# Kernel tuning notes

Measured on AMD Instinct MI355X. Metric: run time of the kernel, lower is better.

## Reference

```python
import jax, jax.numpy as jnp
import numpy as np
import math

D = 768
H = 12
HD = D // H  # 64
B, N = 16, 1024
EPS = 1e-5


def _rope(x, cos, sin):
    # x: [B,N,H,hd]; cos,sin: [1,N,1,hd]
    x1, x2 = x[..., ::2], x[..., 1::2]
    return jnp.concatenate(
        [x1 * cos[..., ::2] - x2 * sin[..., ::2],
         x1 * sin[..., 1::2] + x2 * cos[..., 1::2]], axis=-1)


def setup_inputs() -> dict:
    key = jax.random.key(0)
    ks = jax.random.split(key, 8)
    s = 1.0 / math.sqrt(D)  # xavier-ish scale
    return {
        "x": jax.random.normal(ks[0], (B, N, D), jnp.float32),
        "rope_emb": jax.random.normal(ks[1], (N, HD), jnp.float32),
        "ln_w": jnp.ones((D,), jnp.float32),
        "ln_b": jnp.zeros((D,), jnp.float32),
        "enc_w": jax.random.normal(ks[2], (D, D), jnp.float32) * s,
        "enc_b": jnp.zeros((D,), jnp.float32),
        "qk_w": jax.random.normal(ks[3], (D, D), jnp.float32) * s,
        "qk_b": jnp.zeros((D,), jnp.float32),
        "v_w": jax.random.normal(ks[4], (D, D), jnp.float32) * s,
        "v_b": jnp.zeros((D,), jnp.float32),
        "out_w": jax.random.normal(ks[5], (D, D), jnp.float32) * s,
        "out_b": jnp.zeros((D,), jnp.float32),
        "gate_w": jax.random.normal(ks[6], (D, D), jnp.float32) * s,
        "gate_b": jnp.zeros((D,), jnp.float32),
    }


def reference(x, rope_emb, ln_w, ln_b, enc_w, enc_b, qk_w, qk_b,
              v_w, v_b, out_w, out_b, gate_w, gate_b):
    b, n, d = x.shape
    # Pre-LayerNorm
    mu = jnp.mean(x, axis=-1, keepdims=True)
    var = jnp.mean(jnp.square(x - mu), axis=-1, keepdims=True)
    x_norm = (x - mu) / jnp.sqrt(var + EPS) * ln_w + ln_b
    # sparse latent encoder
    x_latent = jax.nn.relu(x_norm @ enc_w.T + enc_b)
    qk = (x_latent @ qk_w.T + qk_b).reshape(b, n, H, HD)
    v = (x_latent @ v_w.T + v_b).reshape(b, n, H, HD)
    ang = rope_emb[:, :HD]
    cos = jnp.cos(ang)[None, :, None, :]
    sin = jnp.sin(ang)[None, :, None, :]
    qk = _rope(qk, cos, sin)
    # raw (softmax-free) attention, Q=K
    scores = jnp.einsum('bnhd,bmhd->bhnm', qk, qk) / math.sqrt(HD)
    attn = jnp.einsum('bhnm,bmhd->bnhd', scores, v).reshape(b, n, d)
    attn = attn @ out_w.T + out_b
    gate = jax.nn.sigmoid(x_norm @ gate_w.T + gate_b)
    return x + gate * attn
```

## Files before the change

kernel.cpp:

```cpp
#include <hip/hip_runtime.h>

typedef __bf16 bf16;
typedef __bf16 bf16x4 __attribute__((ext_vector_type(4)));
typedef __bf16 bf16x8 __attribute__((ext_vector_type(8)));
typedef float floatx4 __attribute__((ext_vector_type(4)));

#define DD 768
#define NH 12
#define HDIM 64
#define BB 16
#define NN 1024
#define MTOT (BB*NN)
#define WELEM (DD*DD)

#define ABUF 16384
#define BBUF 8192
#define TBUF (ABUF + BBUF)

__device__ __forceinline__ void async_cp16(const void* g, void* l) {
  __builtin_amdgcn_global_load_lds((const __attribute__((address_space(1))) void*)g,
                                   (__attribute__((address_space(3))) void*)l, 16, 0, 0);
}

__global__ __launch_bounds__(256) void ln_kernel(const float* __restrict__ x,
    const float* __restrict__ w, const float* __restrict__ b, bf16* __restrict__ A) {
  int row = blockIdx.x * 4 + (threadIdx.x >> 6);
  int lane = threadIdx.x & 63;
  const float4* xr = (const float4*)(x + (size_t)row * DD);
  float4 v[3];
  float s = 0.f;
#pragma unroll
  for (int i = 0; i < 3; i++) {
    v[i] = xr[lane + 64 * i];
    s += v[i].x + v[i].y + v[i].z + v[i].w;
  }
#pragma unroll
  for (int o = 32; o; o >>= 1) s += __shfl_xor(s, o);
  float mu = s * (1.f / 768.f);
  float vs = 0.f;
#pragma unroll
  for (int i = 0; i < 3; i++) {
    float dx;
    dx = v[i].x - mu; vs += dx * dx;
    dx = v[i].y - mu; vs += dx * dx;
    dx = v[i].z - mu; vs += dx * dx;
    dx = v[i].w - mu; vs += dx * dx;
  }
#pragma unroll
  for (int o = 32; o; o >>= 1) vs += __shfl_xor(vs, o);
  float rstd = rsqrtf(vs * (1.f / 768.f) + 1e-5f);
  const float4* wv = (const float4*)w;
  const float4* bv = (const float4*)b;
  bf16* Ar = A + (size_t)row * DD;
#pragma unroll
  for (int i = 0; i < 3; i++) {
    int c4 = lane + 64 * i;
    float4 ww = wv[c4], bb = bv[c4];
    bf16x4 pk;
    pk[0] = (bf16)((v[i].x - mu) * rstd * ww.x + bb.x);
    pk[1] = (bf16)((v[i].y - mu) * rstd * ww.y + bb.y);
    pk[2] = (bf16)((v[i].z - mu) * rstd * ww.z + bb.z);
    pk[3] = (bf16)((v[i].w - mu) * rstd * ww.w + bb.w);
    *(bf16x4*)(Ar + c4 * 4) = pk;
  }
}

__global__ __launch_bounds__(256) void convw_kernel(const float* __restrict__ w0,
    const float* __restrict__ w1, const float* __restrict__ w2,
    const float* __restrict__ w3, const float* __restrict__ w4, bf16* __restrict__ out) {
  int i = blockIdx.x * 256 + threadIdx.x;
  int which = i / (WELEM / 4);
  int off = (i % (WELEM / 4)) * 4;
  const float* s = which == 0 ? w0 : which == 1 ? w1 : which == 2 ? w2 : which == 3 ? w3 : w4;
  float4 v = *(const float4*)(s + off);
  bf16x4 pk;
  pk[0] = (bf16)v.x; pk[1] = (bf16)v.y; pk[2] = (bf16)v.z; pk[3] = (bf16)v.w;
  *(bf16x4*)(out + (size_t)i * 4) = pk;
}

template<int EPI>
__device__ __forceinline__ void gemm_body(
    int bm, int bn, int bnl,
    const bf16* __restrict__ Aop, const bf16* __restrict__ W,
    const float* __restrict__ bias,
    bf16* __restrict__ Cb, float* __restrict__ Cf,
    const float* __restrict__ Xres, const bf16* __restrict__ Gate,
    bf16* smem) {
  int tid = threadIdx.x;
  int w = tid >> 6, lane = tid & 63;
  int quad = lane >> 4, l16 = lane & 15;
  int wm = w >> 1, wn = w & 1;
  int sr = lane >> 3;
  int scg = (lane & 7) ^ sr;
  int swz = l16 & 7;

  const bf16* Ag = Aop + (size_t)(bm * 256) * DD;
  const bf16* Bg = W + (size_t)(bn * 128) * DD;
  const bf16* srcA = Ag + (size_t)(w * 8 + sr) * DD + scg * 8;
  const bf16* srcB = Bg + (size_t)(w * 8 + sr) * DD + scg * 8;

  floatx4 acc[4][4];
#pragma unroll
  for (int i = 0; i < 4; i++)
#pragma unroll
    for (int j = 0; j < 4; j++)
      acc[i][j] = (floatx4){0.f, 0.f, 0.f, 0.f};

  auto stage = [&](int k0, bf16* buf) {
#pragma unroll
    for (int it = 0; it < 4; it++)
      async_cp16(srcA + (size_t)it * (64 * DD) + k0, buf + (w + 8 * it) * 512);
#pragma unroll
    for (int jt = 0; jt < 2; jt++)
      async_cp16(srcB + (size_t)jt * (64 * DD) + k0, buf + ABUF + (w + 8 * jt) * 512);
  };

  stage(0, smem);
  stage(64, smem + TBUF);

#pragma unroll
  for (int t = 0; t < 12; t++) {
    if (t + 2 < 12) stage((t + 2) * 64, smem + ((t + 2) % 3) * TBUF);
    if (t < 10)       asm volatile("s_waitcnt vmcnt(12)" ::: "memory");
    else if (t == 10) asm volatile("s_waitcnt vmcnt(6)" ::: "memory");
    else              asm volatile("s_waitcnt vmcnt(0)" ::: "memory");
    __builtin_amdgcn_s_barrier();
    __builtin_amdgcn_sched_barrier(0);

    const bf16* Ab = smem + (t % 3) * TBUF;
    const bf16* Bb = Ab + ABUF;
#pragma unroll
    for (int ks = 0; ks < 2; ks++) {
      int cg = (ks * 4 + quad) ^ swz;
      bf16x8 a[4], b[4];
#pragma unroll
      for (int i = 0; i < 4; i++) a[i] = *(const bf16x8*)&Ab[(wm * 64 + i * 16 + l16) * 64 + cg * 8];
#pragma unroll
      for (int i = 0; i < 4; i++) b[i] = *(const bf16x8*)&Bb[(wn * 64 + i * 16 + l16) * 64 + cg * 8];
      __builtin_amdgcn_s_setprio(1);
      if (EPI == 2) {
#pragma unroll
        for (int mi = 0; mi < 4; mi++)
#pragma unroll
          for (int ni = 0; ni < 4; ni++)
            acc[mi][ni] = __builtin_amdgcn_mfma_f32_16x16x32_bf16(a[mi], b[ni], acc[mi][ni], 0, 0, 0);
      } else {
#pragma unroll
        for (int mi = 0; mi < 4; mi++)
#pragma unroll
          for (int ni = 0; ni < 4; ni++)
            acc[mi][ni] = __builtin_amdgcn_mfma_f32_16x16x32_bf16(b[ni], a[mi], acc[mi][ni], 0, 0, 0);
      }
      __builtin_amdgcn_s_setprio(0);
    }
    asm volatile("s_waitcnt lgkmcnt(0)" ::: "memory");
    __builtin_amdgcn_s_barrier();
    __builtin_amdgcn_sched_barrier(0);
  }

  if (EPI == 2) {
#pragma unroll
    for (int ni = 0; ni < 4; ni++) {
      int gc = bnl * 128 + wn * 64 + ni * 16 + l16;
      float bz = bias[gc];
      int h = gc >> 6, dd2 = gc & 63;
#pragma unroll
      for (int mi = 0; mi < 4; mi++) {
        int gm0 = bm * 256 + wm * 64 + mi * 16 + quad * 4;
        int b_ = gm0 >> 10, n0 = gm0 & 1023;
        bf16x4 pk;
#pragma unroll
        for (int r = 0; r < 4; r++) pk[r] = (bf16)(acc[mi][ni][r] + bz);
        *(bf16x4*)&Cb[(((size_t)b_ * NH + h) * HDIM + dd2) * NN + n0] = pk;
      }
    }
  } else {
#pragma unroll
    for (int mi = 0; mi < 4; mi++) {
      int gm = bm * 256 + wm * 64 + mi * 16 + l16;
#pragma unroll
      for (int ni = 0; ni < 4; ni++) {
        int gc = bnl * 128 + wn * 64 + ni * 16 + quad * 4;
        float4 bz = *(const float4*)&bias[gc];
        float v0 = acc[mi][ni][0] + bz.x;
        float v1 = acc[mi][ni][1] + bz.y;
        float v2 = acc[mi][ni][2] + bz.z;
        float v3 = acc[mi][ni][3] + bz.w;
        size_t idx = (size_t)gm * DD + gc;
        if (EPI == 4) {
          bf16x4 g = *(const bf16x4*)&Gate[idx];
          float4 xr = *(const float4*)&Xres[idx];
          float4 o;
          o.x = xr.x + (float)g[0] * v0;
          o.y = xr.y + (float)g[1] * v1;
          o.z = xr.z + (float)g[2] * v2;
          o.w = xr.w + (float)g[3] * v3;
          *(float4*)&Cf[idx] = o;
        } else {
          bf16x4 pk;
          if (EPI == 0) {
            pk[0] = (bf16)fmaxf(v0, 0.f); pk[1] = (bf16)fmaxf(v1, 0.f);
            pk[2] = (bf16)fmaxf(v2, 0.f); pk[3] = (bf16)fmaxf(v3, 0.f);
          } else if (EPI == 1) {
            pk[0] = (bf16)v0; pk[1] = (bf16)v1; pk[2] = (bf16)v2; pk[3] = (bf16)v3;
          } else {
            pk[0] = (bf16)(1.f / (1.f + __expf(-v0)));
            pk[1] = (bf16)(1.f / (1.f + __expf(-v1)));
            pk[2] = (bf16)(1.f / (1.f + __expf(-v2)));
            pk[3] = (bf16)(1.f / (1.f + __expf(-v3)));
          }
          *(bf16x4*)&Cb[idx] = pk;
        }
      }
    }
  }
}

template<int EPI_LO, int EPI_HI, int NBN>
__global__ __launch_bounds__(512, 2) void gemm_kernel(
    const bf16* __restrict__ Aop, const bf16* __restrict__ W,
    const float* __restrict__ bias_lo, const float* __restrict__ bias_hi,
    bf16* __restrict__ C_lo, bf16* __restrict__ C_hi, float* __restrict__ Cf,
    const float* __restrict__ Xres, const bf16* __restrict__ Gate) {
  __shared__ __attribute__((aligned(16))) bf16 smem[3 * TBUF];
  int blk = blockIdx.x;
  int xcd = blk & 7, slot = blk >> 3;
  int bm = xcd * 8 + slot / NBN;
  int bn = slot % NBN;
  if (NBN == 12 && bn >= 6) {
    gemm_body<EPI_HI>(bm, bn, bn - 6, Aop, W, bias_hi, C_hi, Cf, Xres, Gate, smem);
  } else {
    gemm_body<EPI_LO>(bm, bn, bn, Aop, W, bias_lo, C_lo, Cf, Xres, Gate, smem);
  }
}

#define TLS_S 132
__global__ __launch_bounds__(256) void rope_kernel(const bf16* __restrict__ QKraw,
    const float* __restrict__ rope, bf16* __restrict__ QKr, bf16* __restrict__ QKrT) {
  __shared__ bf16 Tls[64 * TLS_S];
  int blk = blockIdx.x;
  int bh = blk >> 3, nc = blk & 7;
  int b_ = bh / NH, h_ = bh % NH;
  int nbase = nc * 128;
  int t = threadIdx.x;
  {
    int n_loc = t >> 1, ch = t & 1;
    int n = nbase + n_loc;
    const bf16* src = QKraw + ((size_t)(b_ * NN + n)) * DD + h_ * HDIM + ch * 32;
    const float* rp = rope + n * HDIM + ch * 32;
    __attribute__((aligned(16))) bf16 o1[16];
    __attribute__((aligned(16))) bf16 o2[16];
#pragma unroll
    for (int i0 = 0; i0 < 4; i0++) {
      bf16x8 v = *(const bf16x8*)(src + i0 * 8);
      float4 r0 = *(const float4*)(rp + i0 * 8);
      float4 r1 = *(const float4*)(rp + i0 * 8 + 4);
      float a0s[4] = {r0.x, r0.z, r1.x, r1.z};
      float a1s[4] = {r0.y, r0.w, r1.y, r1.w};
#pragma unroll
      for (int p = 0; p < 4; p++) {
        float x1 = (float)v[2 * p], x2 = (float)v[2 * p + 1];
        float s0, c0, s1, c1;
        __sincosf(a0s[p], &s0, &c0);
        __sincosf(a1s[p], &s1, &c1);
        int d = i0 * 4 + p;
        o1[d] = (bf16)(x1 * c0 - x2 * s0);
        o2[d] = (bf16)(x1 * s1 + x2 * c1);
      }
    }
    bf16* dst = QKr + ((size_t)(b_ * NN + n)) * DD + h_ * HDIM;
    *(bf16x8*)&dst[ch * 16]      = *(bf16x8*)&o1[0];
    *(bf16x8*)&dst[ch * 16 + 8]  = *(bf16x8*)&o1[8];
    *(bf16x8*)&dst[32 + ch * 16]     = *(bf16x8*)&o2[0];
    *(bf16x8*)&dst[32 + ch * 16 + 8] = *(bf16x8*)&o2[8];
#pragma unroll
    for (int d = 0; d < 16; d++) {
      Tls[(ch * 16 + d) * TLS_S + n_loc] = o1[d];
      Tls[(32 + ch * 16 + d) * TLS_S + n_loc] = o2[d];
    }
  }
  __syncthreads();
  {
    int c = t >> 2, qn = t & 3;
    __attribute__((aligned(16))) bf16 buf[32];
#pragma unroll
    for (int j = 0; j < 8; j++)
      *(bf16x4*)&buf[j * 4] = *(const bf16x4*)&Tls[c * TLS_S + qn * 32 + j * 4];
    bf16* dst = QKrT + ((size_t)bh * HDIM + c) * NN + nbase + qn * 32;
#pragma unroll
    for (int j = 0; j < 4; j++)
      *(bf16x8*)&dst[j * 8] = *(bf16x8*)&buf[j * 8];
  }
}

__global__ __launch_bounds__(256) void attn_kernel(const bf16* __restrict__ QKr,
    const bf16* __restrict__ QKrT, const bf16* __restrict__ VT, bf16* __restrict__ attn) {
  __shared__ float Tp[64][64];
  __shared__ bf16 Tbf[64][72];
  int blk = blockIdx.x;
  int xcd = blk & 7, s = blk >> 3;
  int bhl = s >> 2, q = s & 3;
  int bh = xcd * 24 + bhl;
  int tid = threadIdx.x, wave = tid >> 6, lane = tid & 63;
  int quad = lane >> 4, l16 = lane & 15;
  const bf16* Qt = QKrT + (size_t)bh * (HDIM * NN);
  const bf16* Vt = VT + (size_t)bh * (HDIM * NN);

  floatx4 acc[4][4];
#pragma unroll
  for (int i = 0; i < 4; i++)
#pragma unroll
    for (int j = 0; j < 4; j++)
      acc[i][j] = (floatx4){0.f, 0.f, 0.f, 0.f};

  int kbase = wave * 256;
#pragma unroll
  for (int k0 = 0; k0 < 256; k0 += 32) {
    bf16x8 a[4], b[4];
#pragma unroll
    for (int i = 0; i < 4; i++) a[i] = *(const bf16x8*)&Qt[(size_t)(i * 16 + l16) * NN + kbase + k0 + quad * 8];
#pragma unroll
    for (int i = 0; i < 4; i++) b[i] = *(const bf16x8*)&Vt[(size_t)(i * 16 + l16) * NN + kbase + k0 + quad * 8];
#pragma unroll
    for (int mi = 0; mi < 4; mi++)
#pragma unroll
      for (int ni = 0; ni < 4; ni++)
        acc[mi][ni] = __builtin_amdgcn_mfma_f32_16x16x32_bf16(a[mi], b[ni], acc[mi][ni], 0, 0, 0);
  }
#pragma unroll
  for (int w = 0; w < 4; w++) {
    if (wave == w) {
#pragma unroll
      for (int mi = 0; mi < 4; mi++)
#pragma unroll
        for (int ni = 0; ni < 4; ni++)
#pragma unroll
          for (int r = 0; r < 4; r++) {
            float val = acc[mi][ni][r];
            float* p = &Tp[mi * 16 + quad * 4 + r][ni * 16 + l16];
            if (w == 0) *p = val; else *p += val;
          }
    }
    __syncthreads();
  }
  for (int e = tid; e < 4096; e += 256) {
    int d1 = e >> 6, d2 = e & 63;
    Tbf[d2][d1] = (bf16)(Tp[d1][d2] * 0.125f);
  }
  __syncthreads();

  int b_ = bh / NH, h_ = bh % NH;
  const bf16* Q = QKr + (size_t)(b_ * NN) * DD + h_ * HDIM;
  bf16* Ao = attn + (size_t)(b_ * NN) * DD + h_ * HDIM;
  bf16x8 Bf[4][2];
#pragma unroll
  for (int ni = 0; ni < 4; ni++)
#pragma unroll
    for (int ks = 0; ks < 2; ks++)
      Bf[ni][ks] = *(const bf16x8*)&Tbf[ni * 16 + l16][ks * 32 + quad * 8];

#pragma unroll
  for (int mi = 0; mi < 4; mi++) {
    int nrow = q * 256 + wave * 64 + mi * 16;
    bf16x8 a0 = *(const bf16x8*)&Q[(size_t)(nrow + l16) * DD + quad * 8];
    bf16x8 a1 = *(const bf16x8*)&Q[(size_t)(nrow + l16) * DD + 32 + quad * 8];
    floatx4 o[4];
#pragma unroll
    for (int ni = 0; ni < 4; ni++) o[ni] = (floatx4){0.f, 0.f, 0.f, 0.f};
#pragma unroll
    for (int ni = 0; ni < 4; ni++) {
      o[ni] = __builtin_amdgcn_mfma_f32_16x16x32_bf16(a0, Bf[ni][0], o[ni], 0, 0, 0);
      o[ni] = __builtin_amdgcn_mfma_f32_16x16x32_bf16(a1, Bf[ni][1], o[ni], 0, 0, 0);
    }
#pragma unroll
    for (int ni = 0; ni < 4; ni++)
#pragma unroll
      for (int r = 0; r < 4; r++)
        Ao[(size_t)(nrow + quad * 4 + r) * DD + ni * 16 + l16] = (bf16)o[ni][r];
  }
}

extern "C" void kernel_launch(void* const* d_in, const int* in_sizes, int n_in,
                              void* d_out, int out_size, void* d_ws, size_t ws_size,
                              hipStream_t stream) {
  const float* x      = (const float*)d_in[0];
  const float* rope   = (const float*)d_in[1];
  const float* ln_w   = (const float*)d_in[2];
  const float* ln_b   = (const float*)d_in[3];
  const float* enc_w  = (const float*)d_in[4];
  const float* enc_b  = (const float*)d_in[5];
  const float* qk_w   = (const float*)d_in[6];
  const float* qk_b   = (const float*)d_in[7];
  const float* v_w    = (const float*)d_in[8];
  const float* v_b    = (const float*)d_in[9];
  const float* out_w  = (const float*)d_in[10];
  const float* out_b  = (const float*)d_in[11];
  const float* gate_w = (const float*)d_in[12];
  const float* gate_b = (const float*)d_in[13];

  char* w = (char*)d_ws;
  const size_t S = (size_t)MTOT * DD * 2;
  bf16* s0 = (bf16*)(w);
  bf16* s1 = (bf16*)(w + S);
  bf16* s2 = (bf16*)(w + 2 * S);
  bf16* s3 = (bf16*)(w + 3 * S);
  bf16* s4 = (bf16*)(w + 4 * S);
  bf16* s5 = (bf16*)(w + 5 * S);
  bf16* Wb = (bf16*)(w + 6 * S);

  bf16* A = s0;
  bf16* L = s1;
  bf16* Gate = s2;
  bf16* QKraw = s0;
  bf16* QKr = s3;
  bf16* QKrT = s4;
  bf16* VT = s5;
  bf16* attnb = s1;

  ln_kernel<<<dim3(MTOT / 4), dim3(256), 0, stream>>>(x, ln_w, ln_b, A);
  convw_kernel<<<dim3(5 * WELEM / 4 / 256), dim3(256), 0, stream>>>(enc_w, gate_w, qk_w, v_w, out_w, Wb);

  gemm_kernel<0, 3, 12><<<dim3(768), dim3(512), 0, stream>>>(
      A, Wb, enc_b, gate_b, L, Gate, nullptr, nullptr, nullptr);
  gemm_kernel<1, 2, 12><<<dim3(768), dim3(512), 0, stream>>>(
      L, Wb + 2 * (size_t)WELEM, qk_b, v_b, QKraw, VT, nullptr, nullptr, nullptr);
  rope_kernel<<<dim3(BB * NH * 8), dim3(256), 0, stream>>>(QKraw, rope, QKr, QKrT);
  attn_kernel<<<dim3(BB * NH * 4), dim3(256), 0, stream>>>(QKr, QKrT, VT, attnb);
  gemm_kernel<4, 4, 6><<<dim3(384), dim3(512), 0, stream>>>(
      attnb, Wb + 4 * (size_t)WELEM, out_b, nullptr, nullptr, nullptr, (float*)d_out, x, Gate);
}
```

Baseline: 340.7 us.

## Split GEMM staging across k-steps, merge attention blocks, use simpler out-proj GEMM

```diff
diff --git a/kernel.cpp b/kernel.cpp
--- a/kernel.cpp
+++ b/kernel.cpp
@@ -106,24 +106,24 @@
     for (int j = 0; j < 4; j++)
       acc[i][j] = (floatx4){0.f, 0.f, 0.f, 0.f};
 
-  auto stage = [&](int k0, bf16* buf) {
-#pragma unroll
-    for (int it = 0; it < 4; it++)
-      async_cp16(srcA + (size_t)it * (64 * DD) + k0, buf + (w + 8 * it) * 512);
-#pragma unroll
-    for (int jt = 0; jt < 2; jt++)
-      async_cp16(srcB + (size_t)jt * (64 * DD) + k0, buf + ABUF + (w + 8 * jt) * 512);
+  auto stageH0 = [&](int k0, bf16* buf) {
+    async_cp16(srcA + (size_t)0 * (64 * DD) + k0, buf + (w + 0) * 512);
+    async_cp16(srcA + (size_t)1 * (64 * DD) + k0, buf + (w + 8) * 512);
+    async_cp16(srcB + k0, buf + ABUF + w * 512);
   };
-
-  stage(0, smem);
-  stage(64, smem + TBUF);
+  auto stageH1 = [&](int k0, bf16* buf) {
+    async_cp16(srcA + (size_t)2 * (64 * DD) + k0, buf + (w + 16) * 512);
+    async_cp16(srcA + (size_t)3 * (64 * DD) + k0, buf + (w + 24) * 512);
+    async_cp16(srcB + (size_t)64 * DD + k0, buf + ABUF + (w + 8) * 512);
+  };
+
+  stageH0(0, smem);               stageH1(0, smem);
+  stageH0(64, smem + TBUF);       stageH1(64, smem + TBUF);
 
 #pragma unroll
   for (int t = 0; t < 12; t++) {
-    if (t + 2 < 12) stage((t + 2) * 64, smem + ((t + 2) % 3) * TBUF);
-    if (t < 10)       asm volatile("s_waitcnt vmcnt(12)" ::: "memory");
-    else if (t == 10) asm volatile("s_waitcnt vmcnt(6)" ::: "memory");
-    else              asm volatile("s_waitcnt vmcnt(0)" ::: "memory");
+    if (t < 11) asm volatile("s_waitcnt vmcnt(6)" ::: "memory");
+    else        asm volatile("s_waitcnt vmcnt(0)" ::: "memory");
     __builtin_amdgcn_s_barrier();
     __builtin_amdgcn_sched_barrier(0);
 
@@ -137,6 +137,14 @@
       for (int i = 0; i < 4; i++) a[i] = *(const bf16x8*)&Ab[(wm * 64 + i * 16 + l16) * 64 + cg * 8];
 #pragma unroll
       for (int i = 0; i < 4; i++) b[i] = *(const bf16x8*)&Bb[(wn * 64 + i * 16 + l16) * 64 + cg * 8];
+      if (t < 10) {
+        if (ks == 0) stageH0((t + 2) * 64, smem + ((t + 2) % 3) * TBUF);
+        else         stageH1((t + 2) * 64, smem + ((t + 2) % 3) * TBUF);
+      }
+      __builtin_amdgcn_s_barrier();
+      __builtin_amdgcn_sched_barrier(0);
+      asm volatile("s_waitcnt lgkmcnt(0)" ::: "memory");
+      __builtin_amdgcn_sched_barrier(0);
       __builtin_amdgcn_s_setprio(1);
       if (EPI == 2) {
 #pragma unroll
@@ -153,9 +161,6 @@
       }
       __builtin_amdgcn_s_setprio(0);
     }
-    asm volatile("s_waitcnt lgkmcnt(0)" ::: "memory");
-    __builtin_amdgcn_s_barrier();
-    __builtin_amdgcn_sched_barrier(0);
   }
 
   if (EPI == 2) {
@@ -234,6 +239,109 @@
   }
 }
 
+template<int EPI>
+__device__ __forceinline__ void gemm0_body(
+    int bm, int bn, int bnl,
+    const bf16* __restrict__ Aop, const bf16* __restrict__ W,
+    const float* __restrict__ bias,
+    bf16* __restrict__ Cb, float* __restrict__ Cf,
+    const float* __restrict__ Xres, const bf16* __restrict__ Gate,
+    bf16* As, bf16* Bs) {
+  int tid = threadIdx.x;
+  int wave = tid >> 6, lane = tid & 63;
+  int quad = lane >> 4, l16 = lane & 15;
+  int wm = wave & 1, wn = wave >> 1;
+  int sr = lane >> 3;
+  int smcg = (lane & 7) ^ sr;
+
+  const bf16* Ag = Aop + (size_t)(bm * 256) * DD;
+  const bf16* Bg = W + (size_t)(bn * 128) * DD;
+
+  floatx4 acc[8][4];
+#pragma unroll
+  for (int i = 0; i < 8; i++)
+#pragma unroll
+    for (int j = 0; j < 4; j++)
+      acc[i][j] = (floatx4){0.f, 0.f, 0.f, 0.f};
+
+  int swzA = (l16 & 7);
+
+  for (int k0 = 0; k0 < DD; k0 += 64) {
+    __syncthreads();
+#pragma unroll
+    for (int it = 0; it < 8; it++) {
+      int c = it * 4 + wave;
+      int row = c * 8 + sr;
+      async_cp16(Ag + (size_t)row * DD + k0 + smcg * 8, &As[c * 512]);
+    }
+#pragma unroll
+    for (int it = 0; it < 4; it++) {
+      int c = it * 4 + wave;
+      int row = c * 8 + sr;
+      async_cp16(Bg + (size_t)row * DD + k0 + smcg * 8, &Bs[c * 512]);
+    }
+    __syncthreads();
+#pragma unroll
+    for (int ks = 0; ks < 2; ks++) {
+      int cg = (ks * 4 + quad) ^ swzA;
+      bf16x8 a[8], b[4];
+#pragma unroll
+      for (int i = 0; i < 8; i++) a[i] = *(const bf16x8*)&As[(wm * 128 + i * 16 + l16) * 64 + cg * 8];
+#pragma unroll
+      for (int i = 0; i < 4; i++) b[i] = *(const bf16x8*)&Bs[(wn * 64 + i * 16 + l16) * 64 + cg * 8];
+#pragma unroll
+      for (int mi = 0; mi < 8; mi++)
+#pragma unroll
+        for (int ni = 0; ni < 4; ni++)
+          acc[mi][ni] = __builtin_amdgcn_mfma_f32_16x16x32_bf16(b[ni], a[mi], acc[mi][ni], 0, 0, 0);
+    }
+  }
+
+#pragma unroll
+  for (int mi = 0; mi < 8; mi++) {
+    int gm = bm * 256 + wm * 128 + mi * 16 + l16;
+#pragma unroll
+    for (int ni = 0; ni < 4; ni++) {
+      int gc = bnl * 128 + wn * 64 + ni * 16 + quad * 4;
+      float4 bz = *(const float4*)&bias[gc];
+      float v0 = acc[mi][ni][0] + bz.x;
+      float v1 = acc[mi][ni][1] + bz.y;
+      float v2 = acc[mi][ni][2] + bz.z;
+      float v3 = acc[mi][ni][3] + bz.w;
+      size_t idx = (size_t)gm * DD + gc;
+      if (EPI == 4) {
+        bf16x4 g = *(const bf16x4*)&Gate[idx];
+        float4 xr = *(const float4*)&Xres[idx];
+        float4 o;
+        o.x = xr.x + (float)g[0] * v0;
+        o.y = xr.y + (float)g[1] * v1;
+        o.z = xr.z + (float)g[2] * v2;
+        o.w = xr.w + (float)g[3] * v3;
+        *(float4*)&Cf[idx] = o;
+      } else {
+        bf16x4 pk;
+        pk[0] = (bf16)v0; pk[1] = (bf16)v1; pk[2] = (bf16)v2; pk[3] = (bf16)v3;
+        *(bf16x4*)&Cb[idx] = pk;
+      }
+    }
+  }
+}
+
+template<int EPI, int NBN>
+__global__ __launch_bounds__(256, 2) void gemm0_kernel(
+    const bf16* __restrict__ Aop, const bf16* __restrict__ W,
+    const float* __restrict__ bias,
+    bf16* __restrict__ Cb, float* __restrict__ Cf,
+    const float* __restrict__ Xres, const bf16* __restrict__ Gate) {
+  __shared__ bf16 As[256 * 64];
+  __shared__ bf16 Bs[128 * 64];
+  int blk = blockIdx.x;
+  int xcd = blk & 7, slot = blk >> 3;
+  int bm = xcd * 8 + slot / NBN;
+  int bn = slot % NBN;
+  gemm0_body<EPI>(bm, bn, bn, Aop, W, bias, Cb, Cf, Xres, Gate, As, Bs);
+}
+
 #define TLS_S 132
 __global__ __launch_bounds__(256) void rope_kernel(const bf16* __restrict__ QKraw,
     const float* __restrict__ rope, bf16* __restrict__ QKr, bf16* __restrict__ QKrT) {
@@ -298,8 +406,7 @@
   __shared__ float Tp[64][64];
   __shared__ bf16 Tbf[64][72];
   int blk = blockIdx.x;
-  int xcd = blk & 7, s = blk >> 3;
-  int bhl = s >> 2, q = s & 3;
+  int xcd = blk & 7, bhl = blk >> 3;
   int bh = xcd * 24 + bhl;
   int tid = threadIdx.x, wave = tid >> 6, lane = tid & 63;
   int quad = lane >> 4, l16 = lane & 15;
@@ -360,8 +467,8 @@
       Bf[ni][ks] = *(const bf16x8*)&Tbf[ni * 16 + l16][ks * 32 + quad * 8];
 
 #pragma unroll
-  for (int mi = 0; mi < 4; mi++) {
-    int nrow = q * 256 + wave * 64 + mi * 16;
+  for (int mi = 0; mi < 16; mi++) {
+    int nrow = wave * 256 + mi * 16;
     bf16x8 a0 = *(const bf16x8*)&Q[(size_t)(nrow + l16) * DD + quad * 8];
     bf16x8 a1 = *(const bf16x8*)&Q[(size_t)(nrow + l16) * DD + 32 + quad * 8];
     floatx4 o[4];
@@ -425,7 +532,7 @@
   gemm_kernel<1, 2, 12><<<dim3(768), dim3(512), 0, stream>>>(
       L, Wb + 2 * (size_t)WELEM, qk_b, v_b, QKraw, VT, nullptr, nullptr, nullptr);
   rope_kernel<<<dim3(BB * NH * 8), dim3(256), 0, stream>>>(QKraw, rope, QKr, QKrT);
-  attn_kernel<<<dim3(BB * NH * 4), dim3(256), 0, stream>>>(QKr, QKrT, VT, attnb);
-  gemm_kernel<4, 4, 6><<<dim3(384), dim3(512), 0, stream>>>(
-      attnb, Wb + 4 * (size_t)WELEM, out_b, nullptr, nullptr, nullptr, (float*)d_out, x, Gate);
-}
+  attn_kernel<<<dim3(BB * NH), dim3(256), 0, stream>>>(QKr, QKrT, VT, attnb);
+  gemm0_kernel<4, 6><<<dim3(384), dim3(256), 0, stream>>>(
+      attnb, Wb + 4 * (size_t)WELEM, out_b, nullptr, (float*)d_out, x, Gate);
+}
```

Measured after the change: 336.5 us. No clear change (-1.2%).
